# Kernel optimization log

Measured on AMD Instinct MI355X. Metric: run time of the kernel, lower is better.

## Reference

```python
import jax, jax.numpy as jnp
import numpy as np

CH, KS, PAD = 64, 3, 1
B, H, W = 4, 128, 128
EH, EW = 64, 64
K = KS * KS


def setup_inputs() -> dict:
    key = jax.random.key(0)
    ks = jax.random.split(key, 10)
    C = CH
    z = lambda *s: jnp.zeros(s, jnp.float32)
    return {
        "ev_feat": jax.random.normal(ks[0], (B, C, EH, EW), jnp.float32),
        "im_feat": jax.random.normal(ks[1], (B, C, H, W), jnp.float32),
        "mlp_w0": jax.random.normal(ks[2], (2 * C + 4, C), jnp.float32) * 0.05,
        "mlp_b0": z(C),
        "mlp_w1": jax.random.normal(ks[3], (C, C), jnp.float32) * 0.05,
        "mlp_b1": z(C),
        "mlp_w2": jax.random.normal(ks[4], (C, C), jnp.float32) * 0.05,
        "mlp_b2": z(C),
        "mlp_w3": jax.random.normal(ks[5], (C, C), jnp.float32) * 0.05,
        "mlp_b3": z(C),
        "off_w": jax.random.normal(ks[6], (3 * K, C, KS, KS), jnp.float32) * 0.01,
        "off_b": z(3 * K),
        "dcn_w": jax.random.normal(ks[7], (C, C, KS, KS), jnp.float32) * 0.05,
        "dcn_b": z(C),
    }


def _conv(x, w, b):
    y = jax.lax.conv_general_dilated(x, w, (1, 1), [(PAD, PAD), (PAD, PAD)],
                                     dimension_numbers=("NCHW", "OIHW", "NCHW"))
    return y + b[None, :, None, None]


def _forward(ev_feat, im_feat, mlp_w0, mlp_b0, mlp_w1, mlp_b1, mlp_w2, mlp_b2,
             mlp_w3, mlp_b3, off_w, off_b, dcn_w, dcn_b):
    C = CH
    Bn = im_feat.shape[0]
    Q = H * W
    # ---- coordinate-conditioned MLP: LIIF-style nearest query of ev_feat ----
    ys = -1.0 + (2.0 * jnp.arange(H, dtype=jnp.float32) + 1.0) / H  # pixel centers in [-1,1]
    xs = -1.0 + (2.0 * jnp.arange(W, dtype=jnp.float32) + 1.0) / W
    gy, gx = jnp.meshgrid(ys, xs, indexing="ij")
    coord = jnp.stack([gy, gx], -1).reshape(-1, 2)  # (Q,2) as (y,x), torch make_coord order
    iy = jnp.clip(jnp.round(((coord[:, 0] + 1.0) * EH - 1.0) / 2.0), 0, EH - 1).astype(jnp.int32)
    ix = jnp.clip(jnp.round(((coord[:, 1] + 1.0) * EW - 1.0) / 2.0), 0, EW - 1).astype(jnp.int32)
    q_feat = ev_feat[:, :, iy, ix].transpose(0, 2, 1)  # (B,Q,C) nearest-sampled event feature
    q_coord = jnp.stack([-1.0 + (2.0 * iy + 1.0) / EH, -1.0 + (2.0 * ix + 1.0) / EW], -1)
    rel = (coord - q_coord) * jnp.array([EH, EW], jnp.float32)  # (Q,2) rel coord scaled by feat res
    rel_cell = jnp.array([2.0 / H * EH, 2.0 / W * EW], jnp.float32)  # cell * feat res
    q_im = im_feat.reshape(Bn, C, Q).transpose(0, 2, 1)  # (B,Q,C); coords are im_feat pixel centers
    inp = jnp.concatenate([q_feat, q_im,
                           jnp.broadcast_to(rel, (Bn, Q, 2)),
                           jnp.broadcast_to(rel_cell, (Bn, Q, 2))], -1)  # (B,Q,2C+4)
    x = jax.nn.relu(inp @ mlp_w0 + mlp_b0)
    x = jax.nn.relu(x @ mlp_w1 + mlp_b1)
    x = jax.nn.relu(x @ mlp_w2 + mlp_b2)
    x = x @ mlp_w3 + mlp_b3  # (B,Q,C)
    feat = x.reshape(Bn, H, W, C).transpose(0, 3, 1, 2)  # (B,C,H,W)
    # ---- ModulatedDeformConvPack (DCNv2) ----
    oo = _conv(feat, off_w, off_b)  # (B,3K,H,W)
    o1, o2, m = oo[:, :K], oo[:, K:2 * K], oo[:, 2 * K:]
    off = jnp.concatenate([o1, o2], 1)  # (B,2K,H,W), interleaved (y,x) per kernel tap
    off_y, off_x = off[:, 0::2], off[:, 1::2]  # (B,K,H,W)
    mask = jax.nn.sigmoid(m)  # (B,K,H,W)
    ky = (jnp.arange(K) // KS - PAD).astype(jnp.float32)
    kx = (jnp.arange(K) % KS - PAD).astype(jnp.float32)
    py = jnp.arange(H, dtype=jnp.float32)[None, :, None] + ky[:, None, None] + off_y  # (B,K,H,W)
    px = jnp.arange(W, dtype=jnp.float32)[None, None, :] + kx[:, None, None] + off_x
    y0 = jnp.floor(py)
    x0 = jnp.floor(px)
    ly = py - y0
    lx = px - x0

    def gather(yi, xi):
        valid = (yi >= 0) & (yi <= H - 1) & (xi >= 0) & (xi <= W - 1)
        yc = jnp.clip(yi, 0, H - 1).astype(jnp.int32)
        xc = jnp.clip(xi, 0, W - 1).astype(jnp.int32)
        v = jax.vmap(lambda img, yy, xx: img[:, yy, xx])(feat, yc, xc)  # (B,C,K,H,W)
        return v * valid[:, None].astype(feat.dtype)

    w00 = ((1 - ly) * (1 - lx))[:, None]
    w01 = ((1 - ly) * lx)[:, None]
    w10 = (ly * (1 - lx))[:, None]
    w11 = (ly * lx)[:, None]
    samp = (gather(y0, x0) * w00 + gather(y0, x0 + 1) * w01 +
            gather(y0 + 1, x0) * w10 + gather(y0 + 1, x0 + 1) * w11)  # (B,C,K,H,W)
    samp = samp * mask[:, None]
    out = jnp.einsum("bckhw,ock->bohw", samp, dcn_w.reshape(C, C, K))
    return out + dcn_b[None, :, None, None]


def reference(ev_feat, im_feat, mlp_w0, mlp_b0, mlp_w1, mlp_b1, mlp_w2, mlp_b2,
              mlp_w3, mlp_b3, off_w, off_b, dcn_w, dcn_b):
    return _forward(ev_feat, im_feat, mlp_w0, mlp_b0, mlp_w1, mlp_b1, mlp_w2, mlp_b2,
                    mlp_w3, mlp_b3, off_w, off_b, dcn_w, dcn_b)
```

## Files before the change

### kernel.cpp

```cpp
#include <hip/hip_runtime.h>
#include <math.h>

#define CCH 64
#define HH  128
#define WW  128
#define NB  4
#define NPIX (NB*HH*WW)
#define NWG  (NPIX/64)

__device__ __forceinline__ int swz_block(int bid) {
    return (bid & 7) * (NWG >> 3) + (bid >> 3);
}

__global__ __launch_bounds__(256) void prep_kernel(
    const float* __restrict__ off_w, const float* __restrict__ dcn_w,
    float* __restrict__ offT, float* __restrict__ dcnT)
{
    int idx = blockIdx.x * 256 + threadIdx.x;
    if (idx < 576 * 28) {
        int rc = idx / 28;
        int o  = idx % 28;
        offT[rc * 28 + o] = (o < 27) ? off_w[o * 576 + rc] : 0.0f;
    }
    if (idx < 36864) {
        int o    = idx & 63;
        int rest = idx >> 6;
        int ic   = rest & 63;
        int k    = rest >> 6;
        dcnT[(k * 64 + ic) * 64 + o] = dcn_w[o * 576 + ic * 9 + k];
    }
}

__global__ __launch_bounds__(256) void mlp_kernel(
    const float* __restrict__ ev, const float* __restrict__ im,
    const float* __restrict__ w0, const float* __restrict__ b0,
    const float* __restrict__ w1, const float* __restrict__ b1,
    const float* __restrict__ w2, const float* __restrict__ b2,
    const float* __restrict__ w3, const float* __restrict__ b3,
    float* __restrict__ feat2, float* __restrict__ featN)
{
    __shared__ float xA[64 * 65];
    __shared__ float xB[64 * 65];
    int tid  = threadIdx.x;
    int cg   = __builtin_amdgcn_readfirstlane(tid >> 6);
    int lane = tid & 63;
    int sw   = swz_block(blockIdx.x);
    int p = sw * 64 + lane;
    int b = p >> 14;
    int q = p & 16383;
    int h = q >> 7;
    int w = q & 127;
    int c0 = cg * 16;

    float acc[16];
#pragma unroll
    for (int j = 0; j < 16; ++j) acc[j] = b0[c0 + j];

    const float* evb = ev + ((b * 64) * 64 + (h >> 1)) * 64 + (w >> 1);
    for (int i = 0; i < 64; ++i) {
        float v = evb[i * 4096];
        const float* wr = w0 + i * 64 + c0;
#pragma unroll
        for (int j = 0; j < 16; ++j) acc[j] = fmaf(v, wr[j], acc[j]);
    }
    const float* imb = im + ((b * 64) * 128 + h) * 128 + w;
    for (int i = 0; i < 64; ++i) {
        float v = imb[i * 16384];
        const float* wr = w0 + (64 + i) * 64 + c0;
#pragma unroll
        for (int j = 0; j < 16; ++j) acc[j] = fmaf(v, wr[j], acc[j]);
    }
    {
        float rely = (h & 1) ? 0.5f : -0.5f;
        float relx = (w & 1) ? 0.5f : -0.5f;
        const float* wr = w0 + 128 * 64 + c0;
#pragma unroll
        for (int j = 0; j < 16; ++j) acc[j] = fmaf(rely, wr[j], acc[j]);
#pragma unroll
        for (int j = 0; j < 16; ++j) acc[j] = fmaf(relx, wr[64 + j], acc[j]);
#pragma unroll
        for (int j = 0; j < 16; ++j) acc[j] += wr[128 + j] + wr[192 + j];
    }
#pragma unroll
    for (int j = 0; j < 16; ++j) xA[(c0 + j) * 65 + lane] = fmaxf(acc[j], 0.0f);
    __syncthreads();

#pragma unroll
    for (int j = 0; j < 16; ++j) acc[j] = b1[c0 + j];
    for (int i = 0; i < 64; ++i) {
        float v = xA[i * 65 + lane];
        const float* wr = w1 + i * 64 + c0;
#pragma unroll
        for (int j = 0; j < 16; ++j) acc[j] = fmaf(v, wr[j], acc[j]);
    }
#pragma unroll
    for (int j = 0; j < 16; ++j) xB[(c0 + j) * 65 + lane] = fmaxf(acc[j], 0.0f);
    __syncthreads();

#pragma unroll
    for (int j = 0; j < 16; ++j) acc[j] = b2[c0 + j];
    for (int i = 0; i < 64; ++i) {
        float v = xB[i * 65 + lane];
        const float* wr = w2 + i * 64 + c0;
#pragma unroll
        for (int j = 0; j < 16; ++j) acc[j] = fmaf(v, wr[j], acc[j]);
    }
#pragma unroll
    for (int j = 0; j < 16; ++j) xA[(c0 + j) * 65 + lane] = fmaxf(acc[j], 0.0f);
    __syncthreads();

#pragma unroll
    for (int j = 0; j < 16; ++j) acc[j] = b3[c0 + j];
    for (int i = 0; i < 64; ++i) {
        float v = xA[i * 65 + lane];
        const float* wr = w3 + i * 64 + c0;
#pragma unroll
        for (int j = 0; j < 16; ++j) acc[j] = fmaf(v, wr[j], acc[j]);
    }

    float* fbN = featN + (b * 64 + c0) * 16384 + q;
#pragma unroll
    for (int j = 0; j < 16; ++j) fbN[j * 16384] = acc[j];

#pragma unroll
    for (int j = 0; j < 16; ++j) xB[(c0 + j) * 65 + lane] = acc[j];
    __syncthreads();
    {
        int q0 = (sw * 64) & 16383;
        float* fb = feat2 + ((size_t)b * 16384 + q0) * 64;
        int ch0 = (tid & 15) * 4;
#pragma unroll
        for (int r = 0; r < 4; ++r) {
            int px = (tid >> 4) + r * 16;
            float4 v = make_float4(xB[(ch0 + 0) * 65 + px],
                                   xB[(ch0 + 1) * 65 + px],
                                   xB[(ch0 + 2) * 65 + px],
                                   xB[(ch0 + 3) * 65 + px]);
            ((float4*)fb)[tid + r * 256] = v;
        }
    }
}

__global__ __launch_bounds__(256) void off_kernel(
    const float* __restrict__ featN, const float* __restrict__ offT,
    const float* __restrict__ off_b,
    float* __restrict__ oo)
{
    __shared__ float po[4 * 27 * 64];
    int tid  = threadIdx.x;
    int wv   = __builtin_amdgcn_readfirstlane(tid >> 6);
    int lane = tid & 63;
    int p = swz_block(blockIdx.x) * 64 + lane;
    int b = p >> 14;
    int q = p & 16383;
    int h = q >> 7;
    int w = q & 127;
    int c0 = wv * 16;

    float acc[27];
#pragma unroll
    for (int o = 0; o < 27; ++o) acc[o] = 0.0f;

    const float* fb = featN + (b * 64 + c0) * 16384;
    for (int i = 0; i < 16; ++i) {
        const float* f = fb + i * 16384;
        float v[9];
#pragma unroll
        for (int ky = 0; ky < 3; ++ky)
#pragma unroll
            for (int kx = 0; kx < 3; ++kx) {
                int y = h + ky - 1, x = w + kx - 1;
                bool ok = (y >= 0) && (y < 128) && (x >= 0) && (x < 128);
                v[ky * 3 + kx] = ok ? f[y * 128 + x] : 0.0f;
            }
#pragma unroll
        for (int kk = 0; kk < 9; ++kk) {
            const float* wr = offT + ((c0 + i) * 9 + kk) * 28;
#pragma unroll
            for (int o = 0; o < 27; ++o) acc[o] = fmaf(v[kk], wr[o], acc[o]);
        }
    }

#pragma unroll
    for (int o = 0; o < 27; ++o) po[(wv * 27 + o) * 64 + lane] = acc[o];
    __syncthreads();

#pragma unroll
    for (int j = 0; j < 7; ++j) {
        int o = wv + 4 * j;
        if (o < 27) {
            float s = off_b[o]
                    + po[o * 64 + lane] + po[(27 + o) * 64 + lane]
                    + po[(54 + o) * 64 + lane] + po[(81 + o) * 64 + lane];
            oo[((b * 27 + o) << 14) + q] = s;
        }
    }
}

__device__ __forceinline__ void dcn_transform(
    const float* oob, int k, int h, int w,
    float& W00, float& W01, float& W10, float& W11,
    int& i00, int& i01, int& i10, int& i11)
{
    float oy = oob[(2 * k) << 14];
    float ox = oob[(2 * k + 1) << 14];
    float ml = 1.0f / (1.0f + expf(-oob[(18 + k) << 14]));
    float py = (float)(h + k / 3 - 1) + oy;
    float px = (float)(w + k % 3 - 1) + ox;

    float y0f = floorf(py), x0f = floorf(px);
    float ly = py - y0f, lx = px - x0f;
    int y0 = (int)y0f, x0 = (int)x0f;

    bool vy0 = (y0f >= 0.0f)        && (y0f <= 127.0f);
    bool vy1 = (y0f + 1.0f >= 0.0f) && (y0f + 1.0f <= 127.0f);
    bool vx0 = (x0f >= 0.0f)        && (x0f <= 127.0f);
    bool vx1 = (x0f + 1.0f >= 0.0f) && (x0f + 1.0f <= 127.0f);

    int yc0 = min(max(y0, 0), 127),     yc1 = min(max(y0 + 1, 0), 127);
    int xc0 = min(max(x0, 0), 127),     xc1 = min(max(x0 + 1, 0), 127);

    W00 = (1.0f - ly) * (1.0f - lx) * ml * ((vy0 && vx0) ? 1.0f : 0.0f);
    W01 = (1.0f - ly) * lx          * ml * ((vy0 && vx1) ? 1.0f : 0.0f);
    W10 = ly * (1.0f - lx)          * ml * ((vy1 && vx0) ? 1.0f : 0.0f);
    W11 = ly * lx                   * ml * ((vy1 && vx1) ? 1.0f : 0.0f);

    i00 = yc0 * 128 + xc0; i01 = yc0 * 128 + xc1;
    i10 = yc1 * 128 + xc0; i11 = yc1 * 128 + xc1;
}

__global__ __launch_bounds__(256) void dcn_kernel(
    const float* __restrict__ feat2,
    const float* __restrict__ oo,
    const float* __restrict__ dcnT, const float* __restrict__ dcn_b,
    float* __restrict__ out)
{
    __shared__ float sA[64 * 64];
    __shared__ float sB[64 * 64];
    int tid  = threadIdx.x;
    int wv   = __builtin_amdgcn_readfirstlane(tid >> 6);
    int lane = tid & 63;
    int p = swz_block(blockIdx.x) * 64 + lane;
    int b = p >> 14;
    int q = p & 16383;
    int h = q >> 7;
    int w = q & 127;
    int c0 = wv * 16;

    float acc[16];
#pragma unroll
    for (int j = 0; j < 16; ++j) acc[j] = dcn_b[c0 + j];

    const float* fb2 = feat2 + (b * 16384) * 64 + c0;
    const float* oob = oo + ((b * 27) << 14) + q;

    {
        float W00, W01, W10, W11; int i00, i01, i10, i11;
        dcn_transform(oob, 0, h, w, W00, W01, W10, W11, i00, i01, i10, i11);
        const float4* p00 = (const float4*)(fb2 + i00 * 64);
        const float4* p01 = (const float4*)(fb2 + i01 * 64);
        const float4* p10 = (const float4*)(fb2 + i10 * 64);
        const float4* p11 = (const float4*)(fb2 + i11 * 64);
#pragma unroll
        for (int g = 0; g < 4; ++g) {
            float4 a = p00[g], bb = p01[g], c = p10[g], d = p11[g];
            sA[(c0 + 4 * g + 0) * 64 + lane] = W00 * a.x + W01 * bb.x + W10 * c.x + W11 * d.x;
            sA[(c0 + 4 * g + 1) * 64 + lane] = W00 * a.y + W01 * bb.y + W10 * c.y + W11 * d.y;
            sA[(c0 + 4 * g + 2) * 64 + lane] = W00 * a.z + W01 * bb.z + W10 * c.z + W11 * d.z;
            sA[(c0 + 4 * g + 3) * 64 + lane] = W00 * a.w + W01 * bb.w + W10 * c.w + W11 * d.w;
        }
    }
    __syncthreads();

    float* cur = sA;
    float* nxt = sB;

    for (int k = 0; k < 9; ++k) {
        bool pre = (k < 8);
        float W00, W01, W10, W11; int i00, i01, i10, i11;
        float4 a0, a1, b0, b1, c0v, c1v, d0, d1;
        const float4 *p00 = nullptr, *p01 = nullptr, *p10 = nullptr, *p11 = nullptr;

        if (pre) {
            dcn_transform(oob, k + 1, h, w, W00, W01, W10, W11, i00, i01, i10, i11);
            p00 = (const float4*)(fb2 + i00 * 64);
            p01 = (const float4*)(fb2 + i01 * 64);
            p10 = (const float4*)(fb2 + i10 * 64);
            p11 = (const float4*)(fb2 + i11 * 64);
            a0 = p00[0]; a1 = p00[1];
            b0 = p01[0]; b1 = p01[1];
            c0v = p10[0]; c1v = p10[1];
            d0 = p11[0]; d1 = p11[1];
        }

        const float* wk = dcnT + (k * 64) * 64 + c0;
#pragma unroll 8
        for (int ic = 0; ic < 32; ++ic) {
            float s = cur[ic * 64 + lane];
            const float* wr = wk + ic * 64;
#pragma unroll
            for (int j = 0; j < 16; ++j) acc[j] = fmaf(s, wr[j], acc[j]);
        }

        if (pre) {
            nxt[(c0 + 0) * 64 + lane] = W00 * a0.x + W01 * b0.x + W10 * c0v.x + W11 * d0.x;
            nxt[(c0 + 1) * 64 + lane] = W00 * a0.y + W01 * b0.y + W10 * c0v.y + W11 * d0.y;
            nxt[(c0 + 2) * 64 + lane] = W00 * a0.z + W01 * b0.z + W10 * c0v.z + W11 * d0.z;
            nxt[(c0 + 3) * 64 + lane] = W00 * a0.w + W01 * b0.w + W10 * c0v.w + W11 * d0.w;
            nxt[(c0 + 4) * 64 + lane] = W00 * a1.x + W01 * b1.x + W10 * c1v.x + W11 * d1.x;
            nxt[(c0 + 5) * 64 + lane] = W00 * a1.y + W01 * b1.y + W10 * c1v.y + W11 * d1.y;
            nxt[(c0 + 6) * 64 + lane] = W00 * a1.z + W01 * b1.z + W10 * c1v.z + W11 * d1.z;
            nxt[(c0 + 7) * 64 + lane] = W00 * a1.w + W01 * b1.w + W10 * c1v.w + W11 * d1.w;
            a0 = p00[2]; a1 = p00[3];
            b0 = p01[2]; b1 = p01[3];
            c0v = p10[2]; c1v = p10[3];
            d0 = p11[2]; d1 = p11[3];
        }

#pragma unroll 8
        for (int ic = 32; ic < 64; ++ic) {
            float s = cur[ic * 64 + lane];
            const float* wr = wk + ic * 64;
#pragma unroll
            for (int j = 0; j < 16; ++j) acc[j] = fmaf(s, wr[j], acc[j]);
        }

        if (pre) {
            nxt[(c0 +  8) * 64 + lane] = W00 * a0.x + W01 * b0.x + W10 * c0v.x + W11 * d0.x;
            nxt[(c0 +  9) * 64 + lane] = W00 * a0.y + W01 * b0.y + W10 * c0v.y + W11 * d0.y;
            nxt[(c0 + 10) * 64 + lane] = W00 * a0.z + W01 * b0.z + W10 * c0v.z + W11 * d0.z;
            nxt[(c0 + 11) * 64 + lane] = W00 * a0.w + W01 * b0.w + W10 * c0v.w + W11 * d0.w;
            nxt[(c0 + 12) * 64 + lane] = W00 * a1.x + W01 * b1.x + W10 * c1v.x + W11 * d1.x;
            nxt[(c0 + 13) * 64 + lane] = W00 * a1.y + W01 * b1.y + W10 * c1v.y + W11 * d1.y;
            nxt[(c0 + 14) * 64 + lane] = W00 * a1.z + W01 * b1.z + W10 * c1v.z + W11 * d1.z;
            nxt[(c0 + 15) * 64 + lane] = W00 * a1.w + W01 * b1.w + W10 * c1v.w + W11 * d1.w;
        }

        __syncthreads();
        float* t = cur; cur = nxt; nxt = t;
    }

    float* ob = out + (b * 64 + c0) * 16384 + q;
#pragma unroll
    for (int j = 0; j < 16; ++j) ob[j * 16384] = acc[j];
}

extern "C" void kernel_launch(void* const* d_in, const int* in_sizes, int n_in,
                              void* d_out, int out_size, void* d_ws, size_t ws_size,
                              hipStream_t stream)
{
    const float* ev    = (const float*)d_in[0];
    const float* im    = (const float*)d_in[1];
    const float* w0    = (const float*)d_in[2];
    const float* b0    = (const float*)d_in[3];
    const float* w1    = (const float*)d_in[4];
    const float* b1    = (const float*)d_in[5];
    const float* w2    = (const float*)d_in[6];
    const float* b2    = (const float*)d_in[7];
    const float* w3    = (const float*)d_in[8];
    const float* b3    = (const float*)d_in[9];
    const float* off_w = (const float*)d_in[10];
    const float* off_b = (const float*)d_in[11];
    const float* dcn_w = (const float*)d_in[12];
    const float* dcn_b = (const float*)d_in[13];
    float* out = (float*)d_out;

    char* ws = (char*)d_ws;
    float* feat2 = (float*)(ws);
    float* oo    = (float*)(ws + 16777216);
    float* offT  = (float*)(ws + 23855104);
    float* dcnT  = (float*)(ws + 23920640);
    float* featN = out;

    prep_kernel<<<144, 256, 0, stream>>>(off_w, dcn_w, offT, dcnT);
    mlp_kernel<<<NWG, 256, 0, stream>>>(ev, im, w0, b0, w1, b1, w2, b2,
                                        w3, b3, feat2, featN);
    off_kernel<<<NWG, 256, 0, stream>>>(featN, offT, off_b, oo);
    dcn_kernel<<<NWG, 256, 0, stream>>>(feat2, oo, dcnT, dcn_b, out);
}
```

Baseline: 167.6 us.

## Split DCN reduction over input channels per wave with LDS cross-wave sum

The DCN kernel now has each wave own 16 input channels and accumulate all 64 output channels in registers. Previously the sampled columns were staged through double-buffered LDS, and each wave computed 16 output channels over all 64 inputs. The per-tap LDS exchange and barriers go away; only a final 4-way cross-wave reduction through LDS remains. The 64-float accumulator array raises register pressure and may lower occupancy. Offset loads are also prefetched one tap ahead.

```diff
diff --git a/kernel.cpp b/kernel.cpp
--- a/kernel.cpp
+++ b/kernel.cpp
@@ -197,14 +197,12 @@
     }
 }
 
-__device__ __forceinline__ void dcn_transform(
-    const float* oob, int k, int h, int w,
+__device__ __forceinline__ void dcn_transform_r(
+    float oy, float ox, float mlraw, int k, int h, int w,
     float& W00, float& W01, float& W10, float& W11,
     int& i00, int& i01, int& i10, int& i11)
 {
-    float oy = oob[(2 * k) << 14];
-    float ox = oob[(2 * k + 1) << 14];
-    float ml = 1.0f / (1.0f + expf(-oob[(18 + k) << 14]));
+    float ml = 1.0f / (1.0f + expf(-mlraw));
     float py = (float)(h + k / 3 - 1) + oy;
     float px = (float)(w + k % 3 - 1) + ox;
 
@@ -235,8 +233,7 @@
     const float* __restrict__ dcnT, const float* __restrict__ dcn_b,
     float* __restrict__ out)
 {
-    __shared__ float sA[64 * 64];
-    __shared__ float sB[64 * 64];
+    __shared__ float po[4 * 16 * 64];
     int tid  = threadIdx.x;
     int wv   = __builtin_amdgcn_readfirstlane(tid >> 6);
     int lane = tid & 63;
@@ -247,102 +244,89 @@
     int w = q & 127;
     int c0 = wv * 16;
 
-    float acc[16];
-#pragma unroll
-    for (int j = 0; j < 16; ++j) acc[j] = dcn_b[c0 + j];
-
-    const float* fb2 = feat2 + (b * 16384) * 64 + c0;
+    float acc[64];
+#pragma unroll
+    for (int o = 0; o < 64; ++o) acc[o] = 0.0f;
+
+    const float* fb2 = feat2 + (size_t)(b * 16384) * 64 + c0;
     const float* oob = oo + ((b * 27) << 14) + q;
 
-    {
+    float oyN = oob[0];
+    float oxN = oob[1 << 14];
+    float omN = oob[18 << 14];
+
+    for (int k = 0; k < 9; ++k) {
         float W00, W01, W10, W11; int i00, i01, i10, i11;
-        dcn_transform(oob, 0, h, w, W00, W01, W10, W11, i00, i01, i10, i11);
-        const float4* p00 = (const float4*)(fb2 + i00 * 64);
-        const float4* p01 = (const float4*)(fb2 + i01 * 64);
-        const float4* p10 = (const float4*)(fb2 + i10 * 64);
-        const float4* p11 = (const float4*)(fb2 + i11 * 64);
-#pragma unroll
-        for (int g = 0; g < 4; ++g) {
-            float4 a = p00[g], bb = p01[g], c = p10[g], d = p11[g];
-            sA[(c0 + 4 * g + 0) * 64 + lane] = W00 * a.x + W01 * bb.x + W10 * c.x + W11 * d.x;
-            sA[(c0 + 4 * g + 1) * 64 + lane] = W00 * a.y + W01 * bb.y + W10 * c.y + W11 * d.y;
-            sA[(c0 + 4 * g + 2) * 64 + lane] = W00 * a.z + W01 * bb.z + W10 * c.z + W11 * d.z;
-            sA[(c0 + 4 * g + 3) * 64 + lane] = W00 * a.w + W01 * bb.w + W10 * c.w + W11 * d.w;
-        }
-    }
-    __syncthreads();
-
-    float* cur = sA;
-    float* nxt = sB;
-
-    for (int k = 0; k < 9; ++k) {
-        bool pre = (k < 8);
-        float W00, W01, W10, W11; int i00, i01, i10, i11;
-        float4 a0, a1, b0, b1, c0v, c1v, d0, d1;
-        const float4 *p00 = nullptr, *p01 = nullptr, *p10 = nullptr, *p11 = nullptr;
-
-        if (pre) {
-            dcn_transform(oob, k + 1, h, w, W00, W01, W10, W11, i00, i01, i10, i11);
-            p00 = (const float4*)(fb2 + i00 * 64);
-            p01 = (const float4*)(fb2 + i01 * 64);
-            p10 = (const float4*)(fb2 + i10 * 64);
-            p11 = (const float4*)(fb2 + i11 * 64);
-            a0 = p00[0]; a1 = p00[1];
-            b0 = p01[0]; b1 = p01[1];
-            c0v = p10[0]; c1v = p10[1];
-            d0 = p11[0]; d1 = p11[1];
-        }
-
-        const float* wk = dcnT + (k * 64) * 64 + c0;
-#pragma unroll 8
-        for (int ic = 0; ic < 32; ++ic) {
-            float s = cur[ic * 64 + lane];
-            const float* wr = wk + ic * 64;
-#pragma unroll
-            for (int j = 0; j < 16; ++j) acc[j] = fmaf(s, wr[j], acc[j]);
-        }
-
-        if (pre) {
-            nxt[(c0 + 0) * 64 + lane] = W00 * a0.x + W01 * b0.x + W10 * c0v.x + W11 * d0.x;
-            nxt[(c0 + 1) * 64 + lane] = W00 * a0.y + W01 * b0.y + W10 * c0v.y + W11 * d0.y;
-            nxt[(c0 + 2) * 64 + lane] = W00 * a0.z + W01 * b0.z + W10 * c0v.z + W11 * d0.z;
-            nxt[(c0 + 3) * 64 + lane] = W00 * a0.w + W01 * b0.w + W10 * c0v.w + W11 * d0.w;
-            nxt[(c0 + 4) * 64 + lane] = W00 * a1.x + W01 * b1.x + W10 * c1v.x + W11 * d1.x;
-            nxt[(c0 + 5) * 64 + lane] = W00 * a1.y + W01 * b1.y + W10 * c1v.y + W11 * d1.y;
-            nxt[(c0 + 6) * 64 + lane] = W00 * a1.z + W01 * b1.z + W10 * c1v.z + W11 * d1.z;
-            nxt[(c0 + 7) * 64 + lane] = W00 * a1.w + W01 * b1.w + W10 * c1v.w + W11 * d1.w;
-            a0 = p00[2]; a1 = p00[3];
-            b0 = p01[2]; b1 = p01[3];
-            c0v = p10[2]; c1v = p10[3];
-            d0 = p11[2]; d1 = p11[3];
-        }
-
-#pragma unroll 8
-        for (int ic = 32; ic < 64; ++ic) {
-            float s = cur[ic * 64 + lane];
-            const float* wr = wk + ic * 64;
-#pragma unroll
-            for (int j = 0; j < 16; ++j) acc[j] = fmaf(s, wr[j], acc[j]);
-        }
-
-        if (pre) {
-            nxt[(c0 +  8) * 64 + lane] = W00 * a0.x + W01 * b0.x + W10 * c0v.x + W11 * d0.x;
-            nxt[(c0 +  9) * 64 + lane] = W00 * a0.y + W01 * b0.y + W10 * c0v.y + W11 * d0.y;
-            nxt[(c0 + 10) * 64 + lane] = W00 * a0.z + W01 * b0.z + W10 * c0v.z + W11 * d0.z;
-            nxt[(c0 + 11) * 64 + lane] = W00 * a0.w + W01 * b0.w + W10 * c0v.w + W11 * d0.w;
-            nxt[(c0 + 12) * 64 + lane] = W00 * a1.x + W01 * b1.x + W10 * c1v.x + W11 * d1.x;
-            nxt[(c0 + 13) * 64 + lane] = W00 * a1.y + W01 * b1.y + W10 * c1v.y + W11 * d1.y;
-            nxt[(c0 + 14) * 64 + lane] = W00 * a1.z + W01 * b1.z + W10 * c1v.z + W11 * d1.z;
-            nxt[(c0 + 15) * 64 + lane] = W00 * a1.w + W01 * b1.w + W10 * c1v.w + W11 * d1.w;
-        }
-
+        dcn_transform_r(oyN, oxN, omN, k, h, w, W00, W01, W10, W11,
+                        i00, i01, i10, i11);
+        if (k < 8) {
+            oyN = oob[(2 * (k + 1)) << 14];
+            oxN = oob[(2 * (k + 1) + 1) << 14];
+            omN = oob[(18 + (k + 1)) << 14];
+        }
+
+        float s[16];
+        {
+            const float4* P = (const float4*)(fb2 + i00 * 64);
+            float4 v0 = P[0], v1 = P[1], v2 = P[2], v3 = P[3];
+            s[0]=W00*v0.x; s[1]=W00*v0.y; s[2]=W00*v0.z; s[3]=W00*v0.w;
+            s[4]=W00*v1.x; s[5]=W00*v1.y; s[6]=W00*v1.z; s[7]=W00*v1.w;
+            s[8]=W00*v2.x; s[9]=W00*v2.y; s[10]=W00*v2.z; s[11]=W00*v2.w;
+            s[12]=W00*v3.x; s[13]=W00*v3.y; s[14]=W00*v3.z; s[15]=W00*v3.w;
+        }
+        {
+            const float4* P = (const float4*)(fb2 + i01 * 64);
+            float4 v0 = P[0], v1 = P[1], v2 = P[2], v3 = P[3];
+            s[0]=fmaf(W01,v0.x,s[0]); s[1]=fmaf(W01,v0.y,s[1]); s[2]=fmaf(W01,v0.z,s[2]); s[3]=fmaf(W01,v0.w,s[3]);
+            s[4]=fmaf(W01,v1.x,s[4]); s[5]=fmaf(W01,v1.y,s[5]); s[6]=fmaf(W01,v1.z,s[6]); s[7]=fmaf(W01,v1.w,s[7]);
+            s[8]=fmaf(W01,v2.x,s[8]); s[9]=fmaf(W01,v2.y,s[9]); s[10]=fmaf(W01,v2.z,s[10]); s[11]=fmaf(W01,v2.w,s[11]);
+            s[12]=fmaf(W01,v3.x,s[12]); s[13]=fmaf(W01,v3.y,s[13]); s[14]=fmaf(W01,v3.z,s[14]); s[15]=fmaf(W01,v3.w,s[15]);
+        }
+        {
+            const float4* P = (const float4*)(fb2 + i10 * 64);
+            float4 v0 = P[0], v1 = P[1], v2 = P[2], v3 = P[3];
+            s[0]=fmaf(W10,v0.x,s[0]); s[1]=fmaf(W10,v0.y,s[1]); s[2]=fmaf(W10,v0.z,s[2]); s[3]=fmaf(W10,v0.w,s[3]);
+            s[4]=fmaf(W10,v1.x,s[4]); s[5]=fmaf(W10,v1.y,s[5]); s[6]=fmaf(W10,v1.z,s[6]); s[7]=fmaf(W10,v1.w,s[7]);
+            s[8]=fmaf(W10,v2.x,s[8]); s[9]=fmaf(W10,v2.y,s[9]); s[10]=fmaf(W10,v2.z,s[10]); s[11]=fmaf(W10,v2.w,s[11]);
+            s[12]=fmaf(W10,v3.x,s[12]); s[13]=fmaf(W10,v3.y,s[13]); s[14]=fmaf(W10,v3.z,s[14]); s[15]=fmaf(W10,v3.w,s[15]);
+        }
+        {
+            const float4* P = (const float4*)(fb2 + i11 * 64);
+            float4 v0 = P[0], v1 = P[1], v2 = P[2], v3 = P[3];
+            s[0]=fmaf(W11,v0.x,s[0]); s[1]=fmaf(W11,v0.y,s[1]); s[2]=fmaf(W11,v0.z,s[2]); s[3]=fmaf(W11,v0.w,s[3]);
+            s[4]=fmaf(W11,v1.x,s[4]); s[5]=fmaf(W11,v1.y,s[5]); s[6]=fmaf(W11,v1.z,s[6]); s[7]=fmaf(W11,v1.w,s[7]);
+            s[8]=fmaf(W11,v2.x,s[8]); s[9]=fmaf(W11,v2.y,s[9]); s[10]=fmaf(W11,v2.z,s[10]); s[11]=fmaf(W11,v2.w,s[11]);
+            s[12]=fmaf(W11,v3.x,s[12]); s[13]=fmaf(W11,v3.y,s[13]); s[14]=fmaf(W11,v3.z,s[14]); s[15]=fmaf(W11,v3.w,s[15]);
+        }
+
+        const float* wk = dcnT + (size_t)k * 4096 + c0 * 64;
+#pragma unroll
+        for (int i = 0; i < 16; ++i) {
+            const float* wr = wk + i * 64;
+#pragma unroll
+            for (int o = 0; o < 64; ++o) acc[o] = fmaf(s[i], wr[o], acc[o]);
+        }
+    }
+
+#pragma unroll
+    for (int g = 0; g < 4; ++g) {
+        if (g) __syncthreads();
+#pragma unroll
+        for (int j = 0; j < 16; ++j)
+            po[(wv * 16 + j) * 64 + lane] = acc[g * 16 + j];
         __syncthreads();
-        float* t = cur; cur = nxt; nxt = t;
-    }
-
-    float* ob = out + (b * 64 + c0) * 16384 + q;
-#pragma unroll
-    for (int j = 0; j < 16; ++j) ob[j * 16384] = acc[j];
+#pragma unroll
+        for (int j = 0; j < 4; ++j) {
+            int oj = wv * 4 + j;
+            int o  = g * 16 + oj;
+            float sum = dcn_b[o]
+                      + po[(0 * 16 + oj) * 64 + lane]
+                      + po[(1 * 16 + oj) * 64 + lane]
+                      + po[(2 * 16 + oj) * 64 + lane]
+                      + po[(3 * 16 + oj) * 64 + lane];
+            out[(b * 64 + o) * 16384 + q] = sum;
+        }
+    }
 }
 
 extern "C" void kernel_launch(void* const* d_in, const int* in_sizes, int n_in,
```

Measured after the change: 213.5 us. 1.27x slower.
